# Performance work log

Hardware: AMD Instinct MI355X
Metric: run time of the kernel (lower is better)

Reference implementation:

```python
import jax, jax.numpy as jnp
import numpy as np

N = 200000          # nodes
E = 12_800_000      # edges (avg degree 64)
C = 4               # conv_out_channels == node_features
H = 32              # lstm_out_channels


def setup_inputs() -> dict:
    key = jax.random.key(0)
    ks = jax.random.split(key, 16)
    inv_c = 1.0 / np.sqrt(C)
    inv_h = 1.0 / np.sqrt(H)
    return {
        "x": jax.random.normal(ks[0], (N, C), jnp.float32),
        "edge_index": jax.random.randint(ks[1], (2, E), 0, N, dtype=jnp.int64),
        "edge_weight": jax.random.uniform(ks[2], (E,), jnp.float32),
        "h_0": 0.1 * jax.random.normal(ks[3], (1, N, H), jnp.float32),
        "c_0": 0.1 * jax.random.normal(ks[4], (1, N, H), jnp.float32),
        # GatedGraphConv (num_layers=1): weight[0] of shape [C, C]
        "conv_weight": inv_c * jax.random.normal(ks[5], (C, C), jnp.float32),
        # GRUCell(C, C) params (PyTorch layout: [3C, C], gate order r,z,n)
        "gru_w_ih": inv_c * jax.random.normal(ks[6], (3 * C, C), jnp.float32),
        "gru_w_hh": inv_c * jax.random.normal(ks[7], (3 * C, C), jnp.float32),
        "gru_b_ih": inv_c * jax.random.normal(ks[8], (3 * C,), jnp.float32),
        "gru_b_hh": inv_c * jax.random.normal(ks[9], (3 * C,), jnp.float32),
        # LSTM(C, H, 1 layer) params (PyTorch layout: [4H, *], gate order i,f,g,o)
        "lstm_w_ih": inv_h * jax.random.normal(ks[10], (4 * H, C), jnp.float32),
        "lstm_w_hh": inv_h * jax.random.normal(ks[11], (4 * H, H), jnp.float32),
        "lstm_b_ih": inv_h * jax.random.normal(ks[12], (4 * H,), jnp.float32),
        "lstm_b_hh": inv_h * jax.random.normal(ks[13], (4 * H,), jnp.float32),
        # Linear(32, 1)
        "lin_w": inv_h * jax.random.normal(ks[14], (1, H), jnp.float32),
        "lin_b": inv_h * jax.random.normal(ks[15], (1,), jnp.float32),
    }


def reference(x, edge_index, edge_weight, h_0, c_0,
              conv_weight, gru_w_ih, gru_w_hh, gru_b_ih, gru_b_hh,
              lstm_w_ih, lstm_w_hh, lstm_b_ih, lstm_b_hh, lin_w, lin_b):
    n = x.shape[0]
    src, dst = edge_index[0], edge_index[1]  # source j -> target i

    # ---- GatedGraphConv, 1 layer (in_dim == out_channels, no padding) ----
    m = x @ conv_weight                                   # [N, C]
    msg = m[src] * edge_weight[:, None]                   # [E, C] gather
    summed = jax.ops.segment_sum(msg, dst, num_segments=n)
    cnt = jax.ops.segment_sum(jnp.ones((msg.shape[0],), msg.dtype), dst,
                              num_segments=n)
    agg = summed / jnp.maximum(cnt, 1.0)[:, None]         # mean aggr (empty -> 0)

    # GRUCell(agg, x): r,z,n gate order
    gi = agg @ gru_w_ih.T + gru_b_ih
    gh = x @ gru_w_hh.T + gru_b_hh
    i_r, i_z, i_n = jnp.split(gi, 3, axis=1)
    h_r, h_z, h_n = jnp.split(gh, 3, axis=1)
    r = jax.nn.sigmoid(i_r + h_r)
    z = jax.nn.sigmoid(i_z + h_z)
    nn_ = jnp.tanh(i_n + r * h_n)
    h_conv = (1.0 - z) * nn_ + z * x                      # [N, C]

    # ---- LSTM: seq_len=1, batch=N, 1 layer; gate order i,f,g,o ----
    h_prev, c_prev = h_0[0], c_0[0]                       # [N, H]
    gates = h_conv @ lstm_w_ih.T + lstm_b_ih + h_prev @ lstm_w_hh.T + lstm_b_hh
    ig, fg, gg, og = jnp.split(gates, 4, axis=1)
    ig, fg, og = jax.nn.sigmoid(ig), jax.nn.sigmoid(fg), jax.nn.sigmoid(og)
    gg = jnp.tanh(gg)
    c_new = fg * c_prev + ig * gg
    h_new = og * jnp.tanh(c_new)                          # [N, H]

    # ---- relu + linear head ----
    out = jax.nn.relu(h_new) @ lin_w.T + lin_b            # [N, 1]
    return out, h_new[None], c_new[None]
```

## Files before the change

### kernel.cpp

```cpp
#include <hip/hip_runtime.h>
#include <math.h>

#define B_SHIFT 8
#define BMASK   255
#define CHUNK   16384
#define NTHR    256

#define LDSADD(p, v) __hip_atomic_fetch_add((p), (v), __ATOMIC_RELAXED, \
                                            __HIP_MEMORY_SCOPE_WORKGROUP)

static __device__ __forceinline__ float sigf(float x) {
  return 1.0f / (1.0f + __expf(-x));
}
static __device__ __forceinline__ float tanhfast(float x) {
  return 2.0f / (1.0f + __expf(-2.0f * x)) - 1.0f;
}

__global__ void conv_m_kernel(const float* __restrict__ x,
                              const float* __restrict__ w,
                              float* __restrict__ m, int n) {
  int i = blockIdx.x * blockDim.x + threadIdx.x;
  if (i >= n) return;
  float4 xv = reinterpret_cast<const float4*>(x)[i];
  float4 mv;
  mv.x = xv.x * w[0] + xv.y * w[4] + xv.z * w[8]  + xv.w * w[12];
  mv.y = xv.x * w[1] + xv.y * w[5] + xv.z * w[9]  + xv.w * w[13];
  mv.z = xv.x * w[2] + xv.y * w[6] + xv.z * w[10] + xv.w * w[14];
  mv.w = xv.x * w[3] + xv.y * w[7] + xv.z * w[11] + xv.w * w[15];
  reinterpret_cast<float4*>(m)[i] = mv;
}


__global__ __launch_bounds__(NTHR) void hist_kernel(const int* __restrict__ dst,
                                                    int E, int B,
                                                    int* __restrict__ gCnt) {
  __shared__ int h[1024];
  for (int b = threadIdx.x; b < B; b += NTHR) h[b] = 0;
  __syncthreads();
  const int4* d4 = reinterpret_cast<const int4*>(dst);
  int i4base = (int)(((long long)blockIdx.x * CHUNK) >> 2);
  int lim4 = E >> 2;
#pragma unroll
  for (int j = 0; j < 16; ++j) {
    int i4 = i4base + j * NTHR + threadIdx.x;
    if (i4 < lim4) {
      int4 d = d4[i4];
      atomicAdd(&h[d.x >> B_SHIFT], 1);
      atomicAdd(&h[d.y >> B_SHIFT], 1);
      atomicAdd(&h[d.z >> B_SHIFT], 1);
      atomicAdd(&h[d.w >> B_SHIFT], 1);
    }
  }
  if (blockIdx.x == 0 && threadIdx.x == 0) {
    for (int e = E & ~3; e < E; ++e) atomicAdd(&h[dst[e] >> B_SHIFT], 1);
  }
  __syncthreads();
  for (int b = threadIdx.x; b < B; b += NTHR) {
    int c = h[b];
    if (c) atomicAdd(&gCnt[b], c);
  }
}

__global__ void scan_kernel(const int* __restrict__ gCnt, int B,
                            int* __restrict__ start, int* __restrict__ cursor) {
  __shared__ int s[1024];
  int t = threadIdx.x;
  int v = (t < B) ? gCnt[t] : 0;
  s[t] = v;
  __syncthreads();
  for (int off = 1; off < 1024; off <<= 1) {
    int u = (t >= off) ? s[t - off] : 0;
    __syncthreads();
    s[t] += u;
    __syncthreads();
  }
  if (t < B) {
    int excl = (t == 0) ? 0 : s[t - 1];
    start[t] = excl;
    cursor[t] = excl;
  }
  if (t == 0) start[B] = s[1023];
}

__global__ __launch_bounds__(NTHR) void bin_kernel(const int* __restrict__ ei,
                                                   const float* __restrict__ ew,
                                                   int E, int B,
                                                   int* __restrict__ cursor,
                                                   int2* __restrict__ binned) {
  __shared__ int h[1024];
  for (int b = threadIdx.x; b < B; b += NTHR) h[b] = 0;
  __syncthreads();
  const int* dst = ei + E;
  const int4* d4 = reinterpret_cast<const int4*>(dst);
  const int4* s4 = reinterpret_cast<const int4*>(ei);
  const float4* w4 = reinterpret_cast<const float4*>(ew);
  int i4base = (int)(((long long)blockIdx.x * CHUNK) >> 2);
  int lim4 = E >> 2;
#pragma unroll
  for (int j = 0; j < 16; ++j) {
    int i4 = i4base + j * NTHR + threadIdx.x;
    if (i4 < lim4) {
      int4 d = d4[i4];
      atomicAdd(&h[d.x >> B_SHIFT], 1);
      atomicAdd(&h[d.y >> B_SHIFT], 1);
      atomicAdd(&h[d.z >> B_SHIFT], 1);
      atomicAdd(&h[d.w >> B_SHIFT], 1);
    }
  }
  __syncthreads();
  for (int b = threadIdx.x; b < B; b += NTHR) {
    int c = h[b];
    if (c) h[b] = atomicAdd(&cursor[b], c);
  }
  __syncthreads();
#pragma unroll
  for (int j = 0; j < 16; ++j) {
    int i4 = i4base + j * NTHR + threadIdx.x;
    if (i4 < lim4) {
      int4 d = d4[i4];
      int4 s = s4[i4];
      float4 w = w4[i4];
      int p;
      p = atomicAdd(&h[d.x >> B_SHIFT], 1);
      binned[p] = make_int2((s.x << B_SHIFT) | (d.x & BMASK), __float_as_int(w.x));
      p = atomicAdd(&h[d.y >> B_SHIFT], 1);
      binned[p] = make_int2((s.y << B_SHIFT) | (d.y & BMASK), __float_as_int(w.y));
      p = atomicAdd(&h[d.z >> B_SHIFT], 1);
      binned[p] = make_int2((s.z << B_SHIFT) | (d.z & BMASK), __float_as_int(w.z));
      p = atomicAdd(&h[d.w >> B_SHIFT], 1);
      binned[p] = make_int2((s.w << B_SHIFT) | (d.w & BMASK), __float_as_int(w.w));
    }
  }
  if (blockIdx.x == 0 && threadIdx.x == 0) {
    for (int e = E & ~3; e < E; ++e) {
      int d = dst[e];
      int p = atomicAdd(&cursor[d >> B_SHIFT], 1);
      binned[p] = make_int2((ei[e] << B_SHIFT) | (d & BMASK), __float_as_int(ew[e]));
    }
  }
}

__global__ __launch_bounds__(NTHR) void edge_agg_kernel(
    const float* __restrict__ m, const int2* __restrict__ binned,
    const int* __restrict__ start, float* __restrict__ aggOut, int n) {
  __shared__ float acc[NTHR * 5];
  int tid = threadIdx.x;
#pragma unroll
  for (int k = 0; k < 5; ++k) acc[k * NTHR + tid] = 0.0f;
  __syncthreads();

  int s = start[blockIdx.x], e = start[blockIdx.x + 1];
  const float4* m4 = reinterpret_cast<const float4*>(m);
  int i = s + tid;
  for (; i + 3 * NTHR < e; i += 4 * NTHR) {
    int2 r0 = binned[i];
    int2 r1 = binned[i + NTHR];
    int2 r2 = binned[i + 2 * NTHR];
    int2 r3 = binned[i + 3 * NTHR];
    float4 v0 = m4[r0.x >> B_SHIFT];
    float4 v1 = m4[r1.x >> B_SHIFT];
    float4 v2 = m4[r2.x >> B_SHIFT];
    float4 v3 = m4[r3.x >> B_SHIFT];
    float w0 = __int_as_float(r0.y), w1 = __int_as_float(r1.y);
    float w2 = __int_as_float(r2.y), w3 = __int_as_float(r3.y);
    int a0 = (r0.x & BMASK) * 5, a1 = (r1.x & BMASK) * 5;
    int a2 = (r2.x & BMASK) * 5, a3 = (r3.x & BMASK) * 5;
    LDSADD(&acc[a0 + 0], v0.x * w0); LDSADD(&acc[a0 + 1], v0.y * w0);
    LDSADD(&acc[a0 + 2], v0.z * w0); LDSADD(&acc[a0 + 3], v0.w * w0);
    LDSADD(&acc[a0 + 4], 1.0f);
    LDSADD(&acc[a1 + 0], v1.x * w1); LDSADD(&acc[a1 + 1], v1.y * w1);
    LDSADD(&acc[a1 + 2], v1.z * w1); LDSADD(&acc[a1 + 3], v1.w * w1);
    LDSADD(&acc[a1 + 4], 1.0f);
    LDSADD(&acc[a2 + 0], v2.x * w2); LDSADD(&acc[a2 + 1], v2.y * w2);
    LDSADD(&acc[a2 + 2], v2.z * w2); LDSADD(&acc[a2 + 3], v2.w * w2);
    LDSADD(&acc[a2 + 4], 1.0f);
    LDSADD(&acc[a3 + 0], v3.x * w3); LDSADD(&acc[a3 + 1], v3.y * w3);
    LDSADD(&acc[a3 + 2], v3.z * w3); LDSADD(&acc[a3 + 3], v3.w * w3);
    LDSADD(&acc[a3 + 4], 1.0f);
  }
  for (; i < e; i += NTHR) {
    int2 r = binned[i];
    float4 v = m4[r.x >> B_SHIFT];
    float w = __int_as_float(r.y);
    int a = (r.x & BMASK) * 5;
    LDSADD(&acc[a + 0], v.x * w); LDSADD(&acc[a + 1], v.y * w);
    LDSADD(&acc[a + 2], v.z * w); LDSADD(&acc[a + 3], v.w * w);
    LDSADD(&acc[a + 4], 1.0f);
  }
  __syncthreads();

  int node = (blockIdx.x << B_SHIFT) + tid;
  if (node >= n) return;
  float inv = 1.0f / fmaxf(acc[tid * 5 + 4], 1.0f);
  reinterpret_cast<float4*>(aggOut)[node] =
      make_float4(acc[tid * 5 + 0] * inv, acc[tid * 5 + 1] * inv,
                  acc[tid * 5 + 2] * inv, acc[tid * 5 + 3] * inv);
}

__global__ __launch_bounds__(NTHR) void node_kernel2(
    const float* __restrict__ x, const float* __restrict__ aggIn,
    const float* __restrict__ h0, const float* __restrict__ c0,
    const float* __restrict__ gwi, const float* __restrict__ gwh,
    const float* __restrict__ gbi, const float* __restrict__ gbh,
    const float* __restrict__ lwi, const float* __restrict__ lwh,
    const float* __restrict__ lbi, const float* __restrict__ lbh,
    const float* __restrict__ linw, const float* __restrict__ linb,
    float* __restrict__ out, float* __restrict__ hout, float* __restrict__ cout,
    int n) {
  int i = blockIdx.x * blockDim.x + threadIdx.x;
  if (i >= n) return;
  float4 av = reinterpret_cast<const float4*>(aggIn)[i];
  float agg[4] = {av.x, av.y, av.z, av.w};
  float4 xv = reinterpret_cast<const float4*>(x)[i];
  float xa[4] = {xv.x, xv.y, xv.z, xv.w};

  float hc[4];
#pragma unroll
  for (int c = 0; c < 4; ++c) {
    float gi_r = gbi[c],     gh_r = gbh[c];
    float gi_z = gbi[4 + c], gh_z = gbh[4 + c];
    float gi_n = gbi[8 + c], gh_n = gbh[8 + c];
#pragma unroll
    for (int k = 0; k < 4; ++k) {
      gi_r += agg[k] * gwi[c * 4 + k];       gh_r += xa[k] * gwh[c * 4 + k];
      gi_z += agg[k] * gwi[(4 + c) * 4 + k]; gh_z += xa[k] * gwh[(4 + c) * 4 + k];
      gi_n += agg[k] * gwi[(8 + c) * 4 + k]; gh_n += xa[k] * gwh[(8 + c) * 4 + k];
    }
    float r = sigf(gi_r + gh_r);
    float z = sigf(gi_z + gh_z);
    float nn = tanhfast(gi_n + r * gh_n);
    hc[c] = (1.0f - z) * nn + z * xa[c];
  }

  const float4* h04 = reinterpret_cast<const float4*>(h0) + (size_t)i * 8;
  const float4* c04 = reinterpret_cast<const float4*>(c0) + (size_t)i * 8;
  float hp[32];
#pragma unroll
  for (int q = 0; q < 8; ++q) {
    float4 hv = h04[q];
    hp[q * 4 + 0] = hv.x; hp[q * 4 + 1] = hv.y;
    hp[q * 4 + 2] = hv.z; hp[q * 4 + 3] = hv.w;
  }
  const float4* wih4 = reinterpret_cast<const float4*>(lwi);
  const float4* whh4 = reinterpret_cast<const float4*>(lwh);
  float oacc = linb[0];
  float4* hout4 = reinterpret_cast<float4*>(hout) + (size_t)i * 8;
  float4* cout4 = reinterpret_cast<float4*>(cout) + (size_t)i * 8;

#pragma unroll
  for (int jc = 0; jc < 8; ++jc) {
    float4 cpv = c04[jc];
    float cpa[4] = {cpv.x, cpv.y, cpv.z, cpv.w};
    float hn[4], cn[4];
#pragma unroll
    for (int jj = 0; jj < 4; ++jj) {
      int j = jc * 4 + jj;
      float gI = lbi[j]      + lbh[j];
      float gF = lbi[32 + j] + lbh[32 + j];
      float gG = lbi[64 + j] + lbh[64 + j];
      float gO = lbi[96 + j] + lbh[96 + j];
      float4 wi = wih4[j], wf = wih4[32 + j], wg = wih4[64 + j], wo = wih4[96 + j];
      gI += hc[0] * wi.x + hc[1] * wi.y + hc[2] * wi.z + hc[3] * wi.w;
      gF += hc[0] * wf.x + hc[1] * wf.y + hc[2] * wf.z + hc[3] * wf.w;
      gG += hc[0] * wg.x + hc[1] * wg.y + hc[2] * wg.z + hc[3] * wg.w;
      gO += hc[0] * wo.x + hc[1] * wo.y + hc[2] * wo.z + hc[3] * wo.w;
#pragma unroll
      for (int q = 0; q < 8; ++q) {
        float4 a = whh4[j * 8 + q];
        float4 b = whh4[(32 + j) * 8 + q];
        float4 g = whh4[(64 + j) * 8 + q];
        float4 o = whh4[(96 + j) * 8 + q];
        float p0 = hp[q * 4 + 0], p1 = hp[q * 4 + 1];
        float p2 = hp[q * 4 + 2], p3 = hp[q * 4 + 3];
        gI += p0 * a.x + p1 * a.y + p2 * a.z + p3 * a.w;
        gF += p0 * b.x + p1 * b.y + p2 * b.z + p3 * b.w;
        gG += p0 * g.x + p1 * g.y + p2 * g.z + p3 * g.w;
        gO += p0 * o.x + p1 * o.y + p2 * o.z + p3 * o.w;
      }
      float ig = sigf(gI), fg = sigf(gF), og = sigf(gO), gg = tanhfast(gG);
      float cnew = fg * cpa[jj] + ig * gg;
      float hnew = og * tanhfast(cnew);
      cn[jj] = cnew; hn[jj] = hnew;
      oacc += fmaxf(hnew, 0.0f) * linw[j];
    }
    hout4[jc] = make_float4(hn[0], hn[1], hn[2], hn[3]);
    cout4[jc] = make_float4(cn[0], cn[1], cn[2], cn[3]);
  }
  out[i] = oacc;
}


__global__ void edge_kernel(const int* __restrict__ ei,
                            const float* __restrict__ ew,
                            const float* __restrict__ m,
                            float* __restrict__ summed,
                            float* __restrict__ cnt, int E) {
  int t = blockIdx.x * blockDim.x + threadIdx.x;
  int e0 = t * 4;
  const float4* m4 = reinterpret_cast<const float4*>(m);
  for (int e = e0; e < E && e < e0 + 4; ++e) {
    int s = ei[e], d = ei[E + e];
    float w = ew[e];
    float4 mv = m4[s];
    float* p = summed + 4ll * d;
    unsafeAtomicAdd(p + 0, mv.x * w);
    unsafeAtomicAdd(p + 1, mv.y * w);
    unsafeAtomicAdd(p + 2, mv.z * w);
    unsafeAtomicAdd(p + 3, mv.w * w);
    unsafeAtomicAdd(cnt + d, 1.0f);
  }
}

__global__ __launch_bounds__(NTHR) void node_kernel(
    const float* __restrict__ x, const float* __restrict__ summed,
    const float* __restrict__ cnt,
    const float* __restrict__ h0, const float* __restrict__ c0,
    const float* __restrict__ gwi, const float* __restrict__ gwh,
    const float* __restrict__ gbi, const float* __restrict__ gbh,
    const float* __restrict__ lwi, const float* __restrict__ lwh,
    const float* __restrict__ lbi, const float* __restrict__ lbh,
    const float* __restrict__ linw, const float* __restrict__ linb,
    float* __restrict__ out, float* __restrict__ hout, float* __restrict__ cout,
    int n) {
  int i = blockIdx.x * blockDim.x + threadIdx.x;
  if (i >= n) return;
  float4 sv = reinterpret_cast<const float4*>(summed)[i];
  float inv = 1.0f / fmaxf(cnt[i], 1.0f);
  float agg[4] = {sv.x * inv, sv.y * inv, sv.z * inv, sv.w * inv};
  float4 xv = reinterpret_cast<const float4*>(x)[i];
  float xa[4] = {xv.x, xv.y, xv.z, xv.w};
  float hc[4];
#pragma unroll
  for (int c = 0; c < 4; ++c) {
    float gi_r = gbi[c],     gh_r = gbh[c];
    float gi_z = gbi[4 + c], gh_z = gbh[4 + c];
    float gi_n = gbi[8 + c], gh_n = gbh[8 + c];
#pragma unroll
    for (int k = 0; k < 4; ++k) {
      gi_r += agg[k] * gwi[c * 4 + k];       gh_r += xa[k] * gwh[c * 4 + k];
      gi_z += agg[k] * gwi[(4 + c) * 4 + k]; gh_z += xa[k] * gwh[(4 + c) * 4 + k];
      gi_n += agg[k] * gwi[(8 + c) * 4 + k]; gh_n += xa[k] * gwh[(8 + c) * 4 + k];
    }
    float r = sigf(gi_r + gh_r);
    float z = sigf(gi_z + gh_z);
    float nn = tanhfast(gi_n + r * gh_n);
    hc[c] = (1.0f - z) * nn + z * xa[c];
  }
  const float4* h04 = reinterpret_cast<const float4*>(h0) + (size_t)i * 8;
  const float4* c04 = reinterpret_cast<const float4*>(c0) + (size_t)i * 8;
  float hp[32];
#pragma unroll
  for (int q = 0; q < 8; ++q) {
    float4 hv = h04[q];
    hp[q * 4 + 0] = hv.x; hp[q * 4 + 1] = hv.y;
    hp[q * 4 + 2] = hv.z; hp[q * 4 + 3] = hv.w;
  }
  const float4* wih4 = reinterpret_cast<const float4*>(lwi);
  const float4* whh4 = reinterpret_cast<const float4*>(lwh);
  float oacc = linb[0];
  float4* hout4 = reinterpret_cast<float4*>(hout) + (size_t)i * 8;
  float4* cout4 = reinterpret_cast<float4*>(cout) + (size_t)i * 8;
#pragma unroll
  for (int jc = 0; jc < 8; ++jc) {
    float4 cpv = c04[jc];
    float cpa[4] = {cpv.x, cpv.y, cpv.z, cpv.w};
    float hn[4], cn[4];
#pragma unroll
    for (int jj = 0; jj < 4; ++jj) {
      int j = jc * 4 + jj;
      float gI = lbi[j]      + lbh[j];
      float gF = lbi[32 + j] + lbh[32 + j];
      float gG = lbi[64 + j] + lbh[64 + j];
      float gO = lbi[96 + j] + lbh[96 + j];
      float4 wi = wih4[j], wf = wih4[32 + j], wg = wih4[64 + j], wo = wih4[96 + j];
      gI += hc[0] * wi.x + hc[1] * wi.y + hc[2] * wi.z + hc[3] * wi.w;
      gF += hc[0] * wf.x + hc[1] * wf.y + hc[2] * wf.z + hc[3] * wf.w;
      gG += hc[0] * wg.x + hc[1] * wg.y + hc[2] * wg.z + hc[3] * wg.w;
      gO += hc[0] * wo.x + hc[1] * wo.y + hc[2] * wo.z + hc[3] * wo.w;
#pragma unroll
      for (int q = 0; q < 8; ++q) {
        float4 a = whh4[j * 8 + q];
        float4 b = whh4[(32 + j) * 8 + q];
        float4 g = whh4[(64 + j) * 8 + q];
        float4 o = whh4[(96 + j) * 8 + q];
        float p0 = hp[q * 4 + 0], p1 = hp[q * 4 + 1];
        float p2 = hp[q * 4 + 2], p3 = hp[q * 4 + 3];
        gI += p0 * a.x + p1 * a.y + p2 * a.z + p3 * a.w;
        gF += p0 * b.x + p1 * b.y + p2 * b.z + p3 * b.w;
        gG += p0 * g.x + p1 * g.y + p2 * g.z + p3 * g.w;
        gO += p0 * o.x + p1 * o.y + p2 * o.z + p3 * o.w;
      }
      float ig = sigf(gI), fg = sigf(gF), og = sigf(gO), gg = tanhfast(gG);
      float cnew = fg * cpa[jj] + ig * gg;
      float hnew = og * tanhfast(cnew);
      cn[jj] = cnew; hn[jj] = hnew;
      oacc += fmaxf(hnew, 0.0f) * linw[j];
    }
    hout4[jc] = make_float4(hn[0], hn[1], hn[2], hn[3]);
    cout4[jc] = make_float4(cn[0], cn[1], cn[2], cn[3]);
  }
  out[i] = oacc;
}

extern "C" void kernel_launch(void* const* d_in, const int* in_sizes, int n_in,
                              void* d_out, int out_size, void* d_ws, size_t ws_size,
                              hipStream_t stream) {
  const float* x     = (const float*)d_in[0];
  const int*   ei    = (const int*)d_in[1];
  const float* ew    = (const float*)d_in[2];
  const float* h0    = (const float*)d_in[3];
  const float* c0    = (const float*)d_in[4];
  const float* convw = (const float*)d_in[5];
  const float* gwi   = (const float*)d_in[6];
  const float* gwh   = (const float*)d_in[7];
  const float* gbi   = (const float*)d_in[8];
  const float* gbh   = (const float*)d_in[9];
  const float* lwi   = (const float*)d_in[10];
  const float* lwh   = (const float*)d_in[11];
  const float* lbi   = (const float*)d_in[12];
  const float* lbh   = (const float*)d_in[13];
  const float* linw  = (const float*)d_in[14];
  const float* linb  = (const float*)d_in[15];

  int n = in_sizes[0] / 4;
  int E = in_sizes[1] / 2;

  float* out  = (float*)d_out;
  float* hout = out + n;
  float* cout = hout + (size_t)n * 32;

  int B = (n + BMASK) >> B_SHIFT;
  size_t need = (size_t)E * 8 + (size_t)n * 32 + ((size_t)3 * B + 2) * 4 + 64;

  if (B <= 1024 && ws_size >= need) {
    int2*  binned = (int2*)d_ws;
    float* m      = (float*)(binned + E);
    float* aggOut = m + (size_t)n * 4;
    int*   gCnt   = (int*)(aggOut + (size_t)n * 4);
    int*   start  = gCnt + B;
    int*   cursor = start + B + 1;

    hipMemsetAsync(gCnt, 0, (size_t)B * sizeof(int), stream);
    conv_m_kernel<<<(n + NTHR - 1) / NTHR, NTHR, 0, stream>>>(x, convw, m, n);

    int nbBlocks = (E + CHUNK - 1) / CHUNK;
    hist_kernel<<<nbBlocks, NTHR, 0, stream>>>(ei + E, E, B, gCnt);
    scan_kernel<<<1, 1024, 0, stream>>>(gCnt, B, start, cursor);
    bin_kernel<<<nbBlocks, NTHR, 0, stream>>>(ei, ew, E, B, cursor, binned);

    edge_agg_kernel<<<B, NTHR, 0, stream>>>(m, binned, start, aggOut, n);
    node_kernel2<<<(n + NTHR - 1) / NTHR, NTHR, 0, stream>>>(
        x, aggOut, h0, c0,
        gwi, gwh, gbi, gbh, lwi, lwh, lbi, lbh, linw, linb,
        out, hout, cout, n);
  } else {
    float* m      = (float*)d_ws;
    float* summed = m + (size_t)n * 4;
    float* cntp   = summed + (size_t)n * 4;
    hipMemsetAsync(summed, 0, (size_t)n * 5 * sizeof(float), stream);
    conv_m_kernel<<<(n + NTHR - 1) / NTHR, NTHR, 0, stream>>>(x, convw, m, n);
    int et = (E + 3) / 4;
    edge_kernel<<<(et + NTHR - 1) / NTHR, NTHR, 0, stream>>>(ei, ew, m, summed, cntp, E);
    node_kernel<<<(n + NTHR - 1) / NTHR, NTHR, 0, stream>>>(
        x, summed, cntp, h0, c0,
        gwi, gwh, gbi, gbh, lwi, lwh, lbi, lbh, linw, linb,
        out, hout, cout, n);
  }
}
```

Baseline: 1.157 ms.

## Split edge aggregation across segments, stage LSTM weights in LDS, shrink bin chunks

The edge aggregation kernel now splits each destination bin's edge range across four segments on a second grid dimension, which gives more blocks and parallelism. Each segment flushes its partial sums and counts to global buffers with atomics, and the mean division moves into the node kernel. The node kernel first copies the LSTM and GRU weights into shared memory rather than reading them from global memory for every node, and the gather loop is unrolled eight ways. The histogram and bin chunk size is halved to launch more blocks. Costs added: an extra memset, global float atomics that make summation order nondeterministic, and a per-block weight-staging step.

```diff
diff --git a/kernel.cpp b/kernel.cpp
--- a/kernel.cpp
+++ b/kernel.cpp
@@ -3,8 +3,10 @@
 
 #define B_SHIFT 8
 #define BMASK   255
-#define CHUNK   16384
+#define CHUNK   8192
+#define CITER   (CHUNK / (NTHR * 4))
 #define NTHR    256
+#define SEG     4
 
 #define LDSADD(p, v) __hip_atomic_fetch_add((p), (v), __ATOMIC_RELAXED, \
                                             __HIP_MEMORY_SCOPE_WORKGROUP)
@@ -41,7 +43,7 @@
   int i4base = (int)(((long long)blockIdx.x * CHUNK) >> 2);
   int lim4 = E >> 2;
 #pragma unroll
-  for (int j = 0; j < 16; ++j) {
+  for (int j = 0; j < CITER; ++j) {
     int i4 = i4base + j * NTHR + threadIdx.x;
     if (i4 < lim4) {
       int4 d = d4[i4];
@@ -97,7 +99,7 @@
   int i4base = (int)(((long long)blockIdx.x * CHUNK) >> 2);
   int lim4 = E >> 2;
 #pragma unroll
-  for (int j = 0; j < 16; ++j) {
+  for (int j = 0; j < CITER; ++j) {
     int i4 = i4base + j * NTHR + threadIdx.x;
     if (i4 < lim4) {
       int4 d = d4[i4];
@@ -114,7 +116,7 @@
   }
   __syncthreads();
 #pragma unroll
-  for (int j = 0; j < 16; ++j) {
+  for (int j = 0; j < CITER; ++j) {
     int i4 = i4base + j * NTHR + threadIdx.x;
     if (i4 < lim4) {
       int4 d = d4[i4];
@@ -142,63 +144,69 @@
 
 __global__ __launch_bounds__(NTHR) void edge_agg_kernel(
     const float* __restrict__ m, const int2* __restrict__ binned,
-    const int* __restrict__ start, float* __restrict__ aggOut, int n) {
+    const int* __restrict__ start, float* __restrict__ sumBuf,
+    float* __restrict__ cntBuf, int n) {
   __shared__ float acc[NTHR * 5];
   int tid = threadIdx.x;
+  int b = blockIdx.x;
 #pragma unroll
   for (int k = 0; k < 5; ++k) acc[k * NTHR + tid] = 0.0f;
   __syncthreads();
 
-  int s = start[blockIdx.x], e = start[blockIdx.x + 1];
+  int s0 = start[b], e0 = start[b + 1];
+  int len = e0 - s0;
+  int s = s0 + (int)((long long)len * blockIdx.y / SEG);
+  int e = s0 + (int)((long long)len * (blockIdx.y + 1) / SEG);
+
   const float4* m4 = reinterpret_cast<const float4*>(m);
   int i = s + tid;
-  for (; i + 3 * NTHR < e; i += 4 * NTHR) {
-    int2 r0 = binned[i];
-    int2 r1 = binned[i + NTHR];
-    int2 r2 = binned[i + 2 * NTHR];
-    int2 r3 = binned[i + 3 * NTHR];
-    float4 v0 = m4[r0.x >> B_SHIFT];
-    float4 v1 = m4[r1.x >> B_SHIFT];
-    float4 v2 = m4[r2.x >> B_SHIFT];
-    float4 v3 = m4[r3.x >> B_SHIFT];
-    float w0 = __int_as_float(r0.y), w1 = __int_as_float(r1.y);
-    float w2 = __int_as_float(r2.y), w3 = __int_as_float(r3.y);
-    int a0 = (r0.x & BMASK) * 5, a1 = (r1.x & BMASK) * 5;
-    int a2 = (r2.x & BMASK) * 5, a3 = (r3.x & BMASK) * 5;
-    LDSADD(&acc[a0 + 0], v0.x * w0); LDSADD(&acc[a0 + 1], v0.y * w0);
-    LDSADD(&acc[a0 + 2], v0.z * w0); LDSADD(&acc[a0 + 3], v0.w * w0);
-    LDSADD(&acc[a0 + 4], 1.0f);
-    LDSADD(&acc[a1 + 0], v1.x * w1); LDSADD(&acc[a1 + 1], v1.y * w1);
-    LDSADD(&acc[a1 + 2], v1.z * w1); LDSADD(&acc[a1 + 3], v1.w * w1);
-    LDSADD(&acc[a1 + 4], 1.0f);
-    LDSADD(&acc[a2 + 0], v2.x * w2); LDSADD(&acc[a2 + 1], v2.y * w2);
-    LDSADD(&acc[a2 + 2], v2.z * w2); LDSADD(&acc[a2 + 3], v2.w * w2);
-    LDSADD(&acc[a2 + 4], 1.0f);
-    LDSADD(&acc[a3 + 0], v3.x * w3); LDSADD(&acc[a3 + 1], v3.y * w3);
-    LDSADD(&acc[a3 + 2], v3.z * w3); LDSADD(&acc[a3 + 3], v3.w * w3);
-    LDSADD(&acc[a3 + 4], 1.0f);
+  for (; i + 7 * NTHR < e; i += 8 * NTHR) {
+    int2 r[8];
+    float4 v[8];
+#pragma unroll
+    for (int u = 0; u < 8; ++u) r[u] = binned[i + u * NTHR];
+#pragma unroll
+    for (int u = 0; u < 8; ++u) v[u] = m4[r[u].x >> B_SHIFT];
+#pragma unroll
+    for (int u = 0; u < 8; ++u) {
+      float w = __int_as_float(r[u].y);
+      int a = (r[u].x & BMASK) * 5;
+      LDSADD(&acc[a + 0], v[u].x * w);
+      LDSADD(&acc[a + 1], v[u].y * w);
+      LDSADD(&acc[a + 2], v[u].z * w);
+      LDSADD(&acc[a + 3], v[u].w * w);
+      LDSADD(&acc[a + 4], 1.0f);
+    }
   }
   for (; i < e; i += NTHR) {
     int2 r = binned[i];
     float4 v = m4[r.x >> B_SHIFT];
     float w = __int_as_float(r.y);
     int a = (r.x & BMASK) * 5;
-    LDSADD(&acc[a + 0], v.x * w); LDSADD(&acc[a + 1], v.y * w);
-    LDSADD(&acc[a + 2], v.z * w); LDSADD(&acc[a + 3], v.w * w);
+    LDSADD(&acc[a + 0], v.x * w);
+    LDSADD(&acc[a + 1], v.y * w);
+    LDSADD(&acc[a + 2], v.z * w);
+    LDSADD(&acc[a + 3], v.w * w);
     LDSADD(&acc[a + 4], 1.0f);
   }
   __syncthreads();
 
-  int node = (blockIdx.x << B_SHIFT) + tid;
-  if (node >= n) return;
-  float inv = 1.0f / fmaxf(acc[tid * 5 + 4], 1.0f);
-  reinterpret_cast<float4*>(aggOut)[node] =
-      make_float4(acc[tid * 5 + 0] * inv, acc[tid * 5 + 1] * inv,
-                  acc[tid * 5 + 2] * inv, acc[tid * 5 + 3] * inv);
+  int node = (b << B_SHIFT) + tid;
+  if (node < n) {
+    float c = acc[tid * 5 + 4];
+    if (c != 0.0f) {
+      unsafeAtomicAdd(&sumBuf[(size_t)node * 4 + 0], acc[tid * 5 + 0]);
+      unsafeAtomicAdd(&sumBuf[(size_t)node * 4 + 1], acc[tid * 5 + 1]);
+      unsafeAtomicAdd(&sumBuf[(size_t)node * 4 + 2], acc[tid * 5 + 2]);
+      unsafeAtomicAdd(&sumBuf[(size_t)node * 4 + 3], acc[tid * 5 + 3]);
+      unsafeAtomicAdd(&cntBuf[node], c);
+    }
+  }
 }
 
 __global__ __launch_bounds__(NTHR) void node_kernel2(
-    const float* __restrict__ x, const float* __restrict__ aggIn,
+    const float* __restrict__ x, const float* __restrict__ sumBuf,
+    const float* __restrict__ cntBuf,
     const float* __restrict__ h0, const float* __restrict__ c0,
     const float* __restrict__ gwi, const float* __restrict__ gwh,
     const float* __restrict__ gbi, const float* __restrict__ gbh,
@@ -207,24 +215,41 @@
     const float* __restrict__ linw, const float* __restrict__ linb,
     float* __restrict__ out, float* __restrict__ hout, float* __restrict__ cout,
     int n) {
-  int i = blockIdx.x * blockDim.x + threadIdx.x;
+  __shared__ float4 s_lwh[1024];
+  __shared__ float4 s_lwi[128];
+  __shared__ float  s_lb[128];
+  __shared__ float  s_linw[32];
+  __shared__ float  s_gwi[48], s_gwh[48], s_gbi[12], s_gbh[12];
+
+  int tid = threadIdx.x;
+  for (int k = tid; k < 4096; k += NTHR) ((float*)s_lwh)[k] = lwh[k];
+  for (int k = tid; k < 512; k += NTHR) ((float*)s_lwi)[k] = lwi[k];
+  if (tid < 128) s_lb[tid] = lbi[tid] + lbh[tid];
+  if (tid < 32) s_linw[tid] = linw[tid];
+  if (tid < 48) { s_gwi[tid] = gwi[tid]; s_gwh[tid] = gwh[tid]; }
+  if (tid < 12) { s_gbi[tid] = gbi[tid]; s_gbh[tid] = gbh[tid]; }
+  __syncthreads();
+
+  int i = blockIdx.x * blockDim.x + tid;
   if (i >= n) return;
-  float4 av = reinterpret_cast<const float4*>(aggIn)[i];
-  float agg[4] = {av.x, av.y, av.z, av.w};
+
+  float4 sv = reinterpret_cast<const float4*>(sumBuf)[i];
+  float inv = 1.0f / fmaxf(cntBuf[i], 1.0f);
+  float agg[4] = {sv.x * inv, sv.y * inv, sv.z * inv, sv.w * inv};
   float4 xv = reinterpret_cast<const float4*>(x)[i];
   float xa[4] = {xv.x, xv.y, xv.z, xv.w};
 
   float hc[4];
 #pragma unroll
   for (int c = 0; c < 4; ++c) {
-    float gi_r = gbi[c],     gh_r = gbh[c];
-    float gi_z = gbi[4 + c], gh_z = gbh[4 + c];
-    float gi_n = gbi[8 + c], gh_n = gbh[8 + c];
+    float gi_r = s_gbi[c],     gh_r = s_gbh[c];
+    float gi_z = s_gbi[4 + c], gh_z = s_gbh[4 + c];
+    float gi_n = s_gbi[8 + c], gh_n = s_gbh[8 + c];
 #pragma unroll
     for (int k = 0; k < 4; ++k) {
-      gi_r += agg[k] * gwi[c * 4 + k];       gh_r += xa[k] * gwh[c * 4 + k];
-      gi_z += agg[k] * gwi[(4 + c) * 4 + k]; gh_z += xa[k] * gwh[(4 + c) * 4 + k];
-      gi_n += agg[k] * gwi[(8 + c) * 4 + k]; gh_n += xa[k] * gwh[(8 + c) * 4 + k];
+      gi_r += agg[k] * s_gwi[c * 4 + k];       gh_r += xa[k] * s_gwh[c * 4 + k];
+      gi_z += agg[k] * s_gwi[(4 + c) * 4 + k]; gh_z += xa[k] * s_gwh[(4 + c) * 4 + k];
+      gi_n += agg[k] * s_gwi[(8 + c) * 4 + k]; gh_n += xa[k] * s_gwh[(8 + c) * 4 + k];
     }
     float r = sigf(gi_r + gh_r);
     float z = sigf(gi_z + gh_z);
@@ -241,8 +266,6 @@
     hp[q * 4 + 0] = hv.x; hp[q * 4 + 1] = hv.y;
     hp[q * 4 + 2] = hv.z; hp[q * 4 + 3] = hv.w;
   }
-  const float4* wih4 = reinterpret_cast<const float4*>(lwi);
-  const float4* whh4 = reinterpret_cast<const float4*>(lwh);
   float oacc = linb[0];
   float4* hout4 = reinterpret_cast<float4*>(hout) + (size_t)i * 8;
   float4* cout4 = reinterpret_cast<float4*>(cout) + (size_t)i * 8;
@@ -255,21 +278,21 @@
 #pragma unroll
     for (int jj = 0; jj < 4; ++jj) {
       int j = jc * 4 + jj;
-      float gI = lbi[j]      + lbh[j];
-      float gF = lbi[32 + j] + lbh[32 + j];
-      float gG = lbi[64 + j] + lbh[64 + j];
-      float gO = lbi[96 + j] + lbh[96 + j];
-      float4 wi = wih4[j], wf = wih4[32 + j], wg = wih4[64 + j], wo = wih4[96 + j];
+      float gI = s_lb[j];
+      float gF = s_lb[32 + j];
+      float gG = s_lb[64 + j];
+      float gO = s_lb[96 + j];
+      float4 wi = s_lwi[j], wf = s_lwi[32 + j], wg = s_lwi[64 + j], wo = s_lwi[96 + j];
       gI += hc[0] * wi.x + hc[1] * wi.y + hc[2] * wi.z + hc[3] * wi.w;
       gF += hc[0] * wf.x + hc[1] * wf.y + hc[2] * wf.z + hc[3] * wf.w;
       gG += hc[0] * wg.x + hc[1] * wg.y + hc[2] * wg.z + hc[3] * wg.w;
       gO += hc[0] * wo.x + hc[1] * wo.y + hc[2] * wo.z + hc[3] * wo.w;
 #pragma unroll
       for (int q = 0; q < 8; ++q) {
-        float4 a = whh4[j * 8 + q];
-        float4 b = whh4[(32 + j) * 8 + q];
-        float4 g = whh4[(64 + j) * 8 + q];
-        float4 o = whh4[(96 + j) * 8 + q];
+        float4 a = s_lwh[j * 8 + q];
+        float4 b = s_lwh[(32 + j) * 8 + q];
+        float4 g = s_lwh[(64 + j) * 8 + q];
+        float4 o = s_lwh[(96 + j) * 8 + q];
         float p0 = hp[q * 4 + 0], p1 = hp[q * 4 + 1];
         float p2 = hp[q * 4 + 2], p3 = hp[q * 4 + 3];
         gI += p0 * a.x + p1 * a.y + p2 * a.z + p3 * a.w;
@@ -281,7 +304,7 @@
       float cnew = fg * cpa[jj] + ig * gg;
       float hnew = og * tanhfast(cnew);
       cn[jj] = cnew; hn[jj] = hnew;
-      oacc += fmaxf(hnew, 0.0f) * linw[j];
+      oacc += fmaxf(hnew, 0.0f) * s_linw[j];
     }
     hout4[jc] = make_float4(hn[0], hn[1], hn[2], hn[3]);
     cout4[jc] = make_float4(cn[0], cn[1], cn[2], cn[3]);
@@ -430,17 +453,19 @@
   float* cout = hout + (size_t)n * 32;
 
   int B = (n + BMASK) >> B_SHIFT;
-  size_t need = (size_t)E * 8 + (size_t)n * 32 + ((size_t)3 * B + 2) * 4 + 64;
+  size_t need = (size_t)E * 8 + (size_t)n * 36 + ((size_t)3 * B + 2) * 4 + 64;
 
   if (B <= 1024 && ws_size >= need) {
     int2*  binned = (int2*)d_ws;
     float* m      = (float*)(binned + E);
-    float* aggOut = m + (size_t)n * 4;
-    int*   gCnt   = (int*)(aggOut + (size_t)n * 4);
+    float* sumBuf = m + (size_t)n * 4;
+    float* cntBuf = sumBuf + (size_t)n * 4;
+    int*   gCnt   = (int*)(cntBuf + n);
     int*   start  = gCnt + B;
     int*   cursor = start + B + 1;
 
     hipMemsetAsync(gCnt, 0, (size_t)B * sizeof(int), stream);
+    hipMemsetAsync(sumBuf, 0, (size_t)n * 5 * sizeof(float), stream);
     conv_m_kernel<<<(n + NTHR - 1) / NTHR, NTHR, 0, stream>>>(x, convw, m, n);
 
     int nbBlocks = (E + CHUNK - 1) / CHUNK;
@@ -448,9 +473,10 @@
     scan_kernel<<<1, 1024, 0, stream>>>(gCnt, B, start, cursor);
     bin_kernel<<<nbBlocks, NTHR, 0, stream>>>(ei, ew, E, B, cursor, binned);
 
-    edge_agg_kernel<<<B, NTHR, 0, stream>>>(m, binned, start, aggOut, n);
+    edge_agg_kernel<<<dim3(B, SEG), NTHR, 0, stream>>>(m, binned, start,
+                                                       sumBuf, cntBuf, n);
     node_kernel2<<<(n + NTHR - 1) / NTHR, NTHR, 0, stream>>>(
-        x, aggOut, h0, c0,
+        x, sumBuf, cntBuf, h0, c0,
         gwi, gwh, gbi, gbh, lwi, lwh, lbi, lbh, linw, linb,
         out, hout, cout, n);
   } else {
```

New measurement: 955.8 us. 17.4% less time.
